# Kernel optimization log

Measured on AMD Instinct MI355X. Metric: run time of the kernel, lower is better.

Reference implementation:

```python
import jax, jax.numpy as jnp
import numpy as np

N_USERS = 100000
N_ITEMS = 40000
DIM = 64
NNZ_UI = 1500000
NNZ_II = 1000000
NNZ_UU = 1500000
UI_LAYERS = 3
ITEM_LAYERS = 2
USER_LAYERS = 2
EPS = 1e-12


def spmm(rows, cols, vals, x, n_rows):
    # sparse COO matrix (rows, cols, vals) @ dense x -> [n_rows, d]
    return jax.ops.segment_sum(vals[:, None] * x[cols], rows, num_segments=n_rows)


def l2_normalize(x):
    # matches F.normalize(x, p=2, dim=1) with eps clamp
    n = jnp.linalg.norm(x, axis=1, keepdims=True)
    return x / jnp.maximum(n, EPS)


def setup_inputs() -> dict:
    key = jax.random.key(0)
    ks = jax.random.split(key, 13)
    N = N_USERS + N_ITEMS
    return {
        "user_ui_emb": jax.random.normal(ks[0], (N_USERS, DIM), jnp.float32) * 0.1,
        "item_ui_emb": jax.random.normal(ks[1], (N_ITEMS, DIM), jnp.float32) * 0.1,
        "uu_emb": jax.random.normal(ks[2], (N_USERS, DIM), jnp.float32) * 0.1,
        "ii_emb": jax.random.normal(ks[3], (N_ITEMS, DIM), jnp.float32) * 0.1,
        "ui_vals": jax.random.uniform(ks[4], (NNZ_UI,), jnp.float32) / 12.0,
        "ii_vals": jax.random.uniform(ks[5], (NNZ_II,), jnp.float32) / 25.0,
        "uu_vals": jax.random.uniform(ks[6], (NNZ_UU,), jnp.float32) / 15.0,
        "ui_rows": jax.random.randint(ks[7], (NNZ_UI,), 0, N, jnp.int32),
        "ui_cols": jax.random.randint(ks[8], (NNZ_UI,), 0, N, jnp.int32),
        "ii_rows": jax.random.randint(ks[9], (NNZ_II,), 0, N_ITEMS, jnp.int32),
        "ii_cols": jax.random.randint(ks[10], (NNZ_II,), 0, N_ITEMS, jnp.int32),
        "uu_rows": jax.random.randint(ks[11], (NNZ_UU,), 0, N_USERS, jnp.int32),
        "uu_cols": jax.random.randint(ks[12], (NNZ_UU,), 0, N_USERS, jnp.int32),
    }


def reference(user_ui_emb, item_ui_emb, uu_emb, ii_emb,
              ui_vals, ii_vals, uu_vals,
              ui_rows, ui_cols, ii_rows, ii_cols, uu_rows, uu_cols):
    N = N_USERS + N_ITEMS
    # II propagation (item_loss_ratio != 0)
    ii = ii_emb
    for _ in range(ITEM_LAYERS):
        ii = spmm(ii_rows, ii_cols, ii_vals, ii, N_ITEMS)
    # UU propagation (user_loss_ratio != 0)
    uu = uu_emb
    for _ in range(USER_LAYERS):
        uu = spmm(uu_rows, uu_cols, uu_vals, uu, N_USERS)
    # LightGCN UI propagation
    ego = jnp.concatenate([user_ui_emb, item_ui_emb], axis=0)  # [N, d]
    acc = ego
    for _ in range(UI_LAYERS):
        ego = spmm(ui_rows, ui_cols, ui_vals, ego, N)
        acc = acc + ego
    all_emb = acc / (UI_LAYERS + 1)  # mean over stacked layers
    u_ui_emb = all_emb[:N_USERS]
    i_ui_emb = all_emb[N_USERS:]
    i_ui_emb = i_ui_emb + l2_normalize(ii)
    u_ui_emb = u_ui_emb + l2_normalize(uu)
    return (u_ui_emb, i_ui_emb, ii, uu)
```

## Files before the change

kernel.cpp:

```cpp
#include <hip/hip_runtime.h>

#define N_USERS_C 100000
#define N_ITEMS_C 40000
#define NTOT_C    140000
#define DIM_C     64
#define CDIV(a, b) (((a) + (b) - 1) / (b))

__device__ __forceinline__ unsigned short f2bf(float f) {
    unsigned u = __float_as_uint(f);
    unsigned r = (u + 0x7FFFu + ((u >> 16) & 1u)) >> 16;
    return (unsigned short)r;
}


template <int LOG_BR>
__global__ __launch_bounds__(256) void bucket_hist(
    const int* __restrict__ rows, int row_off, int* __restrict__ bkt_count,
    int nnz, int NB) {
    __shared__ int cnt[256];
    if (threadIdx.x < NB) cnt[threadIdx.x] = 0;
    __syncthreads();
    for (int e = blockIdx.x * 256 + threadIdx.x; e < nnz; e += gridDim.x * 256)
        atomicAdd(&cnt[(rows[e] + row_off) >> LOG_BR], 1);
    __syncthreads();
    if (threadIdx.x < NB) {
        int c = cnt[threadIdx.x];
        if (c) atomicAdd(&bkt_count[threadIdx.x], c);
    }
}

__global__ __launch_bounds__(256) void bucket_scan(
    const int* __restrict__ bkt_count, int* __restrict__ bkt_start,
    int* __restrict__ bkt_cursor, int NB, int nnz) {
    __shared__ int s[256];
    int v = (threadIdx.x < NB) ? bkt_count[threadIdx.x] : 0;
    s[threadIdx.x] = v;
    __syncthreads();
    #pragma unroll
    for (int off = 1; off < 256; off <<= 1) {
        int t = (threadIdx.x >= off) ? s[threadIdx.x - off] : 0;
        __syncthreads();
        s[threadIdx.x] += t;
        __syncthreads();
    }
    if (threadIdx.x < NB) {
        int ex = s[threadIdx.x] - v;
        bkt_start[threadIdx.x] = ex;
        bkt_cursor[threadIdx.x] = ex;
    }
    if (threadIdx.x == 0) bkt_start[NB] = nnz;
}

template <int LOG_BR>
__global__ __launch_bounds__(256) void partition_edges(
    const int* __restrict__ rows, const int* __restrict__ cols,
    const float* __restrict__ vals, int row_off, int col_off,
    int* __restrict__ bkt_cursor, int2* __restrict__ inter, int nnz) {
    __shared__ int cnt[256];
    __shared__ int base[256];
    const int tile = blockIdx.x * 4096;
    cnt[threadIdx.x] = 0;
    __syncthreads();
    int myrow[16];
    #pragma unroll
    for (int i = 0; i < 16; ++i) {
        int e = tile + i * 256 + threadIdx.x;
        int r = (e < nnz) ? (rows[e] + row_off) : -1;
        myrow[i] = r;
        if (r >= 0) atomicAdd(&cnt[r >> LOG_BR], 1);
    }
    __syncthreads();
    {
        int c = cnt[threadIdx.x];
        if (c) base[threadIdx.x] = atomicAdd(&bkt_cursor[threadIdx.x], c);
        cnt[threadIdx.x] = 0;
    }
    __syncthreads();
    #pragma unroll
    for (int i = 0; i < 16; ++i) {
        int r = myrow[i];
        if (r < 0) continue;
        int b = r >> LOG_BR;
        int rank = atomicAdd(&cnt[b], 1);
        int e = tile + i * 256 + threadIdx.x;
        int rl = r & ((1 << LOG_BR) - 1);
        inter[base[b] + rank] = make_int2((rl << 18) | (cols[e] + col_off),
                                          __float_as_int(vals[e]));
    }
}

template <int LOG_BR, int THREADS>
__global__ __launch_bounds__(THREADS) void bucket_to_csr(
    const int* __restrict__ bkt_start, const int2* __restrict__ inter,
    int2* __restrict__ spack, int* __restrict__ rowptr, int n_rows, int nnz) {
    const int BR = 1 << LOG_BR;
    const int C = BR / THREADS;
    __shared__ int hist[BR];
    __shared__ int bsum[THREADS];
    const int b = blockIdx.x;
    const int lo = bkt_start[b], hi = bkt_start[b + 1];
    #pragma unroll
    for (int j = 0; j < C; ++j) hist[threadIdx.x * C + j] = 0;
    __syncthreads();
    for (int i = lo + threadIdx.x; i < hi; i += THREADS)
        atomicAdd(&hist[inter[i].x >> 18], 1);
    __syncthreads();
    int loc[4];
    int sum = 0;
    #pragma unroll
    for (int j = 0; j < C; ++j) { loc[j] = sum; sum += hist[threadIdx.x * C + j]; }
    bsum[threadIdx.x] = sum;
    __syncthreads();
    #pragma unroll
    for (int off = 1; off < THREADS; off <<= 1) {
        int t = (threadIdx.x >= off) ? bsum[threadIdx.x - off] : 0;
        __syncthreads();
        bsum[threadIdx.x] += t;
        __syncthreads();
    }
    int texcl = bsum[threadIdx.x] - sum;
    __syncthreads();
    #pragma unroll
    for (int j = 0; j < C; ++j) {
        int r = threadIdx.x * C + j;
        int abs0 = lo + texcl + loc[j];
        int grow = (b << LOG_BR) + r;
        if (grow < n_rows) rowptr[grow] = abs0;
        hist[r] = abs0;
    }
    if (b == gridDim.x - 1 && threadIdx.x == 0) rowptr[n_rows] = nnz;
    __syncthreads();
    for (int i = lo + threadIdx.x; i < hi; i += THREADS) {
        int2 p = inter[i];
        int pos = atomicAdd(&hist[p.x >> 18], 1);
        spack[pos] = make_int2(p.x & 0x3FFFF, p.y);
    }
}

__global__ __launch_bounds__(256) void concat2_to_bf16(
    const float* __restrict__ A, const float* __restrict__ B, int n4A,
    int n4tot, unsigned short* __restrict__ dst) {
    int gid = blockIdx.x * blockDim.x + threadIdx.x;
    if (gid >= n4tot) return;
    float4 v = (gid < n4A) ? ((const float4*)A)[gid] : ((const float4*)B)[gid - n4A];
    ushort4 o;
    o.x = f2bf(v.x); o.y = f2bf(v.y); o.z = f2bf(v.z); o.w = f2bf(v.w);
    ((ushort4*)dst)[gid] = o;
}

template <int MODE>
__global__ __launch_bounds__(256, 6) void spmm_csr4(
    const int* __restrict__ rowptr, const int2* __restrict__ spack,
    const unsigned short* __restrict__ x, unsigned short* __restrict__ out_bf,
    float* __restrict__ out_f32, float* __restrict__ acc,
    const float* __restrict__ ego_u, const float* __restrict__ ego_i,
    int n_rows, int nnz) {
    const int wq   = (blockIdx.x * 256 + threadIdx.x) >> 6;
    const int lane = threadIdx.x & 63;
    const int l    = lane & 15;
    const int row  = wq * 4 + (lane >> 4);

    int j = rowptr[row];
    int e = rowptr[row + 1];
    int rem = e - j;
    int m1 = max(rem, __shfl_xor(rem, 16, 64));
    int mrem = max(m1, __shfl_xor(m1, 32, 64));

    const uint2* __restrict__ xq = (const uint2*)x;
    const int last = nnz - 1;

    float4 sa[4];
    #pragma unroll
    for (int u = 0; u < 4; ++u) sa[u] = make_float4(0.f, 0.f, 0.f, 0.f);

    if (mrem > 0) {
        int base = j;
        int2 pA[4], pB[4];
        #pragma unroll
        for (int u = 0; u < 4; ++u) pA[u] = spack[min(base + u, last)];
        #pragma unroll
        for (int u = 0; u < 4; ++u) pB[u] = spack[min(base + 4 + u, last)];
        uint2 gA[4], gB[4];
        #pragma unroll
        for (int u = 0; u < 4; ++u)
            gA[u] = xq[(u < rem) ? ((pA[u].x << 4) + l) : l];
        for (;;) {
            {
                int remN = rem - 4;
                #pragma unroll
                for (int u = 0; u < 4; ++u)
                    gB[u] = xq[(u < remN) ? ((pB[u].x << 4) + l) : l];
                float v[4];
                #pragma unroll
                for (int u = 0; u < 4; ++u)
                    v[u] = (u < rem) ? __int_as_float(pA[u].y) : 0.f;
                #pragma unroll
                for (int u = 0; u < 4; ++u)
                    pA[u] = spack[min(base + 8 + u, last)];
                #pragma unroll
                for (int u = 0; u < 4; ++u) {
                    sa[u].x += v[u] * __uint_as_float(gA[u].x << 16);
                    sa[u].y += v[u] * __uint_as_float(gA[u].x & 0xFFFF0000u);
                    sa[u].z += v[u] * __uint_as_float(gA[u].y << 16);
                    sa[u].w += v[u] * __uint_as_float(gA[u].y & 0xFFFF0000u);
                }
            }
            mrem -= 4;
            if (mrem <= 0) break;
            rem -= 4;
            base += 4;
            {
                int remN = rem - 4;
                #pragma unroll
                for (int u = 0; u < 4; ++u)
                    gA[u] = xq[(u < remN) ? ((pA[u].x << 4) + l) : l];
                float v[4];
                #pragma unroll
                for (int u = 0; u < 4; ++u)
                    v[u] = (u < rem) ? __int_as_float(pB[u].y) : 0.f;
                #pragma unroll
                for (int u = 0; u < 4; ++u)
                    pB[u] = spack[min(base + 8 + u, last)];
                #pragma unroll
                for (int u = 0; u < 4; ++u) {
                    sa[u].x += v[u] * __uint_as_float(gB[u].x << 16);
                    sa[u].y += v[u] * __uint_as_float(gB[u].x & 0xFFFF0000u);
                    sa[u].z += v[u] * __uint_as_float(gB[u].y << 16);
                    sa[u].w += v[u] * __uint_as_float(gB[u].y & 0xFFFF0000u);
                }
            }
            mrem -= 4;
            if (mrem <= 0) break;
            rem -= 4;
            base += 4;
        }
    }
    float4 s;
    s.x = (sa[0].x + sa[1].x) + (sa[2].x + sa[3].x);
    s.y = (sa[0].y + sa[1].y) + (sa[2].y + sa[3].y);
    s.z = (sa[0].z + sa[1].z) + (sa[2].z + sa[3].z);
    s.w = (sa[0].w + sa[1].w) + (sa[2].w + sa[3].w);

    const size_t idx4 = (size_t)row * 16 + l;
    if (MODE == 0 || MODE == 1 || MODE == 2) {
        ushort4 o;
        o.x = f2bf(s.x); o.y = f2bf(s.y); o.z = f2bf(s.z); o.w = f2bf(s.w);
        ((ushort4*)out_bf)[idx4] = o;
    }
    if (MODE == 1) {
        float4 e4 = (row < N_USERS_C)
            ? ((const float4*)ego_u)[idx4]
            : ((const float4*)ego_i)[(size_t)(row - N_USERS_C) * 16 + l];
        ((float4*)acc)[idx4] = make_float4(e4.x + s.x, e4.y + s.y,
                                           e4.z + s.z, e4.w + s.w);
    } else if (MODE == 2 || MODE == 3) {
        float4 a = ((const float4*)acc)[idx4];
        ((float4*)acc)[idx4] = make_float4(a.x + s.x, a.y + s.y,
                                           a.z + s.z, a.w + s.w);
    } else if (MODE == 4 || MODE == 5) {
        ((float4*)out_f32)[idx4] = s;
        float ss = s.x * s.x + s.y * s.y + s.z * s.z + s.w * s.w;
        #pragma unroll
        for (int off = 1; off < 16; off <<= 1) ss += __shfl_xor(ss, off, 64);
        float inv = 1.f / fmaxf(sqrtf(ss), 1e-12f);
        size_t aidx = idx4;
        if (MODE == 5) {
            int arow = (row < N_ITEMS_C) ? (N_USERS_C + row) : (row - N_ITEMS_C);
            aidx = (size_t)arow * 16 + l;
        }
        float4 a = ((const float4*)acc)[aidx];
        a.x = a.x * 0.25f + s.x * inv;
        a.y = a.y * 0.25f + s.y * inv;
        a.z = a.z * 0.25f + s.z * inv;
        a.w = a.w * 0.25f + s.w * inv;
        ((float4*)acc)[aidx] = a;
    }
}


template <int MODE>
static inline void run_spmm(const int* rowptr, const int2* spack,
                            const unsigned short* x, unsigned short* out_bf,
                            float* out_f32, float* acc, const float* ego_u,
                            const float* ego_i, int n_rows, int nnz, hipStream_t s) {
    spmm_csr4<MODE><<<n_rows / 16, 256, 0, s>>>(rowptr, spack, x, out_bf, out_f32,
                                                acc, ego_u, ego_i, n_rows, nnz);
}

extern "C" void kernel_launch(void* const* d_in, const int* in_sizes, int n_in,
                              void* d_out, int out_size, void* d_ws, size_t ws_size,
                              hipStream_t stream) {
    const float* user_ui = (const float*)d_in[0];
    const float* item_ui = (const float*)d_in[1];
    const float* uu_emb  = (const float*)d_in[2];
    const float* ii_emb  = (const float*)d_in[3];
    const float* ui_vals = (const float*)d_in[4];
    const float* ii_vals = (const float*)d_in[5];
    const float* uu_vals = (const float*)d_in[6];
    const int* ui_rows = (const int*)d_in[7];
    const int* ui_cols = (const int*)d_in[8];
    const int* ii_rows = (const int*)d_in[9];
    const int* ii_cols = (const int*)d_in[10];
    const int* uu_rows = (const int*)d_in[11];
    const int* uu_cols = (const int*)d_in[12];
    const int nnz_ui = in_sizes[4];
    const int nnz_ii = in_sizes[5];
    const int nnz_uu = in_sizes[6];
    const int nnz_cat = nnz_ii + nnz_uu;

    float* out    = (float*)d_out;
    float* acc    = out;
    float* acc_u  = acc;
    float* acc_i  = acc + (size_t)N_USERS_C * DIM_C;
    float* out_ii = out + (size_t)NTOT_C * DIM_C;
    float* out_uu = out_ii + (size_t)N_ITEMS_C * DIM_C;
    float* out_cat = out_ii;

    const size_t buf_bytes = (size_t)NTOT_C * DIM_C * sizeof(unsigned short);
    const size_t sp_ui  = (size_t)nnz_ui * sizeof(int2);
    const size_t sp_cat = (size_t)nnz_cat * sizeof(int2);
    const size_t meta_bytes = ((size_t)(NTOT_C + 1) + 1024) * sizeof(int);

    size_t slotA = sp_cat > sp_ui ? sp_cat : sp_ui;
    size_t slotB = slotA > buf_bytes ? slotA : buf_bytes;
    bool use_cat = ws_size >= slotA + slotB + buf_bytes + meta_bytes;
    if (!use_cat) {
        size_t mx = sp_ui;
        if ((size_t)nnz_ii * sizeof(int2) > mx) mx = (size_t)nnz_ii * sizeof(int2);
        if ((size_t)nnz_uu * sizeof(int2) > mx) mx = (size_t)nnz_uu * sizeof(int2);
        slotA = mx;
        slotB = buf_bytes;
    }

    char* p = (char*)d_ws;
    int2* spack = (int2*)p;                     p += slotA;
    int2* inter = (int2*)p;
    unsigned short* buf0 = (unsigned short*)p;  p += slotB;
    unsigned short* buf1 = (unsigned short*)p;  p += buf_bytes;
    int* rowptr     = (int*)p;
    int* bkt_count  = rowptr + (NTOT_C + 1);
    int* bkt_start  = bkt_count + 257;
    int* bkt_cursor = bkt_start + 258;

    const int n4tot = NTOT_C * DIM_C / 4;
    const int n4u   = N_USERS_C * DIM_C / 4;
    const int n4i   = N_ITEMS_C * DIM_C / 4;

    {
        const int NB = (NTOT_C + 1023) >> 10;
        hipMemsetAsync(bkt_count, 0, (size_t)NB * sizeof(int), stream);
        bucket_hist<10><<<512, 256, 0, stream>>>(ui_rows, 0, bkt_count, nnz_ui, NB);
        bucket_scan<<<1, 256, 0, stream>>>(bkt_count, bkt_start, bkt_cursor, NB, nnz_ui);
        partition_edges<10><<<(nnz_ui + 4095) / 4096, 256, 0, stream>>>(
            ui_rows, ui_cols, ui_vals, 0, 0, bkt_cursor, inter, nnz_ui);
        bucket_to_csr<10, 1024><<<NB, 1024, 0, stream>>>(bkt_start, inter, spack,
                                                         rowptr, NTOT_C, nnz_ui);
    }
    concat2_to_bf16<<<(n4tot + 255) / 256, 256, 0, stream>>>(user_ui, item_ui,
                                                             n4u, n4tot, buf1);
    run_spmm<1>(rowptr, spack, buf1, buf0, nullptr, acc, user_ui, item_ui,
                NTOT_C, nnz_ui, stream);
    run_spmm<2>(rowptr, spack, buf0, buf1, nullptr, acc, nullptr, nullptr,
                NTOT_C, nnz_ui, stream);
    run_spmm<3>(rowptr, spack, buf1, nullptr, nullptr, acc, nullptr, nullptr,
                NTOT_C, nnz_ui, stream);

    if (use_cat) {
        const int NB = (NTOT_C + 1023) >> 10;
        hipMemsetAsync(bkt_count, 0, (size_t)NB * sizeof(int), stream);
        bucket_hist<10><<<512, 256, 0, stream>>>(ii_rows, 0, bkt_count, nnz_ii, NB);
        bucket_hist<10><<<512, 256, 0, stream>>>(uu_rows, N_ITEMS_C, bkt_count,
                                                 nnz_uu, NB);
        bucket_scan<<<1, 256, 0, stream>>>(bkt_count, bkt_start, bkt_cursor, NB,
                                           nnz_cat);
        partition_edges<10><<<(nnz_ii + 4095) / 4096, 256, 0, stream>>>(
            ii_rows, ii_cols, ii_vals, 0, 0, bkt_cursor, inter, nnz_ii);
        partition_edges<10><<<(nnz_uu + 4095) / 4096, 256, 0, stream>>>(
            uu_rows, uu_cols, uu_vals, N_ITEMS_C, N_ITEMS_C, bkt_cursor, inter,
            nnz_uu);
        bucket_to_csr<10, 1024><<<NB, 1024, 0, stream>>>(bkt_start, inter, spack,
                                                         rowptr, NTOT_C, nnz_cat);
        concat2_to_bf16<<<(n4tot + 255) / 256, 256, 0, stream>>>(ii_emb, uu_emb,
                                                                 n4i, n4tot, buf1);
        run_spmm<0>(rowptr, spack, buf1, buf0, nullptr, nullptr, nullptr, nullptr,
                    NTOT_C, nnz_cat, stream);
        run_spmm<5>(rowptr, spack, buf0, nullptr, out_cat, acc, nullptr, nullptr,
                    NTOT_C, nnz_cat, stream);
    } else {
        {
            const int NB = (N_ITEMS_C + 255) >> 8;
            hipMemsetAsync(bkt_count, 0, (size_t)NB * sizeof(int), stream);
            bucket_hist<8><<<512, 256, 0, stream>>>(ii_rows, 0, bkt_count, nnz_ii, NB);
            bucket_scan<<<1, 256, 0, stream>>>(bkt_count, bkt_start, bkt_cursor,
                                               NB, nnz_ii);
            partition_edges<8><<<(nnz_ii + 4095) / 4096, 256, 0, stream>>>(
                ii_rows, ii_cols, ii_vals, 0, 0, bkt_cursor, inter, nnz_ii);
            bucket_to_csr<8, 256><<<NB, 256, 0, stream>>>(bkt_start, inter, spack,
                                                          rowptr, N_ITEMS_C, nnz_ii);
        }
        concat2_to_bf16<<<(n4i + 255) / 256, 256, 0, stream>>>(ii_emb, ii_emb,
                                                               n4i, n4i, buf0);
        run_spmm<0>(rowptr, spack, buf0, buf1, nullptr, nullptr, nullptr, nullptr,
                    N_ITEMS_C, nnz_ii, stream);
        run_spmm<4>(rowptr, spack, buf1, nullptr, out_ii, acc_i, nullptr, nullptr,
                    N_ITEMS_C, nnz_ii, stream);
        {
            const int NB = (N_USERS_C + 511) >> 9;
            hipMemsetAsync(bkt_count, 0, (size_t)NB * sizeof(int), stream);
            bucket_hist<9><<<512, 256, 0, stream>>>(uu_rows, 0, bkt_count, nnz_uu, NB);
            bucket_scan<<<1, 256, 0, stream>>>(bkt_count, bkt_start, bkt_cursor,
                                               NB, nnz_uu);
            partition_edges<9><<<(nnz_uu + 4095) / 4096, 256, 0, stream>>>(
                uu_rows, uu_cols, uu_vals, 0, 0, bkt_cursor, inter, nnz_uu);
            bucket_to_csr<9, 256><<<NB, 256, 0, stream>>>(bkt_start, inter, spack,
                                                          rowptr, N_USERS_C, nnz_uu);
        }
        concat2_to_bf16<<<(n4u + 255) / 256, 256, 0, stream>>>(uu_emb, uu_emb,
                                                               n4u, n4u, buf0);
        run_spmm<0>(rowptr, spack, buf0, buf1, nullptr, nullptr, nullptr, nullptr,
                    N_USERS_C, nnz_uu, stream);
        run_spmm<4>(rowptr, spack, buf1, nullptr, out_uu, acc_u, nullptr, nullptr,
                    N_USERS_C, nnz_uu, stream);
    }
}
```

Baseline: 613.7 us.

## Sort rows by degree for SpMM wave balance and pad edge array to drop clamps

Adds a degree histogram and scatter pass that builds a permutation ordering rows by descending degree (capped at 255). The SpMM kernel then maps each 16-lane group to a permuted row, so the four rows sharing a wavefront have similar lengths and less divergence from the max-remaining loop. It also zero-pads the packed edge array so the per-load min clamps and masked gather indices can be removed. The cost is extra small kernels per graph build, an indirect row lookup, and scattered output writes.

After: 1.458 ms. 2.38x slower.

```diff
diff --git a/kernel.cpp b/kernel.cpp
--- a/kernel.cpp
+++ b/kernel.cpp
@@ -4,6 +4,7 @@
 #define N_ITEMS_C 40000
 #define NTOT_C    140000
 #define DIM_C     64
+#define SPAD      256
 #define CDIV(a, b) (((a) + (b) - 1) / (b))
 
 __device__ __forceinline__ unsigned short f2bf(float f) {
@@ -137,6 +138,30 @@
     }
 }
 
+__global__ __launch_bounds__(256) void deg_hist(
+    const int* __restrict__ rowptr, int n, int* __restrict__ dhist) {
+    __shared__ int h[256];
+    h[threadIdx.x] = 0;
+    __syncthreads();
+    for (int i = blockIdx.x * 256 + threadIdx.x; i < n; i += gridDim.x * 256) {
+        int d = rowptr[i + 1] - rowptr[i];
+        atomicAdd(&h[255 - min(d, 255)], 1);
+    }
+    __syncthreads();
+    int c = h[threadIdx.x];
+    if (c) atomicAdd(&dhist[threadIdx.x], c);
+}
+
+__global__ __launch_bounds__(256) void deg_scatter(
+    const int* __restrict__ rowptr, int n, int* __restrict__ dcur,
+    int* __restrict__ perm) {
+    int i = blockIdx.x * 256 + threadIdx.x;
+    if (i >= n) return;
+    int d = rowptr[i + 1] - rowptr[i];
+    int pos = atomicAdd(&dcur[255 - min(d, 255)], 1);
+    perm[pos] = i;
+}
+
 __global__ __launch_bounds__(256) void concat2_to_bf16(
     const float* __restrict__ A, const float* __restrict__ B, int n4A,
     int n4tot, unsigned short* __restrict__ dst) {
@@ -150,15 +175,15 @@
 
 template <int MODE>
 __global__ __launch_bounds__(256, 6) void spmm_csr4(
-    const int* __restrict__ rowptr, const int2* __restrict__ spack,
-    const unsigned short* __restrict__ x, unsigned short* __restrict__ out_bf,
-    float* __restrict__ out_f32, float* __restrict__ acc,
-    const float* __restrict__ ego_u, const float* __restrict__ ego_i,
-    int n_rows, int nnz) {
+    const int* __restrict__ rowptr, const int* __restrict__ perm,
+    const int2* __restrict__ spack, const unsigned short* __restrict__ x,
+    unsigned short* __restrict__ out_bf, float* __restrict__ out_f32,
+    float* __restrict__ acc, const float* __restrict__ ego_u,
+    const float* __restrict__ ego_i) {
     const int wq   = (blockIdx.x * 256 + threadIdx.x) >> 6;
     const int lane = threadIdx.x & 63;
     const int l    = lane & 15;
-    const int row  = wq * 4 + (lane >> 4);
+    const int row  = perm[wq * 4 + (lane >> 4)];
 
     int j = rowptr[row];
     int e = rowptr[row + 1];
@@ -167,7 +192,6 @@
     int mrem = max(m1, __shfl_xor(m1, 32, 64));
 
     const uint2* __restrict__ xq = (const uint2*)x;
-    const int last = nnz - 1;
 
     float4 sa[4];
     #pragma unroll
@@ -177,26 +201,22 @@
         int base = j;
         int2 pA[4], pB[4];
         #pragma unroll
-        for (int u = 0; u < 4; ++u) pA[u] = spack[min(base + u, last)];
+        for (int u = 0; u < 4; ++u) pA[u] = spack[base + u];
         #pragma unroll
-        for (int u = 0; u < 4; ++u) pB[u] = spack[min(base + 4 + u, last)];
+        for (int u = 0; u < 4; ++u) pB[u] = spack[base + 4 + u];
         uint2 gA[4], gB[4];
         #pragma unroll
-        for (int u = 0; u < 4; ++u)
-            gA[u] = xq[(u < rem) ? ((pA[u].x << 4) + l) : l];
+        for (int u = 0; u < 4; ++u) gA[u] = xq[(pA[u].x << 4) + l];
         for (;;) {
             {
-                int remN = rem - 4;
-                #pragma unroll
-                for (int u = 0; u < 4; ++u)
-                    gB[u] = xq[(u < remN) ? ((pB[u].x << 4) + l) : l];
+                #pragma unroll
+                for (int u = 0; u < 4; ++u) gB[u] = xq[(pB[u].x << 4) + l];
                 float v[4];
                 #pragma unroll
                 for (int u = 0; u < 4; ++u)
                     v[u] = (u < rem) ? __int_as_float(pA[u].y) : 0.f;
                 #pragma unroll
-                for (int u = 0; u < 4; ++u)
-                    pA[u] = spack[min(base + 8 + u, last)];
+                for (int u = 0; u < 4; ++u) pA[u] = spack[base + 8 + u];
                 #pragma unroll
                 for (int u = 0; u < 4; ++u) {
                     sa[u].x += v[u] * __uint_as_float(gA[u].x << 16);
@@ -210,17 +230,14 @@
             rem -= 4;
             base += 4;
             {
-                int remN = rem - 4;
-                #pragma unroll
-                for (int u = 0; u < 4; ++u)
-                    gA[u] = xq[(u < remN) ? ((pA[u].x << 4) + l) : l];
+                #pragma unroll
+                for (int u = 0; u < 4; ++u) gA[u] = xq[(pA[u].x << 4) + l];
                 float v[4];
                 #pragma unroll
                 for (int u = 0; u < 4; ++u)
                     v[u] = (u < rem) ? __int_as_float(pB[u].y) : 0.f;
                 #pragma unroll
-                for (int u = 0; u < 4; ++u)
-                    pB[u] = spack[min(base + 8 + u, last)];
+                for (int u = 0; u < 4; ++u) pB[u] = spack[base + 8 + u];
                 #pragma unroll
                 for (int u = 0; u < 4; ++u) {
                     sa[u].x += v[u] * __uint_as_float(gB[u].x << 16);
@@ -279,12 +296,21 @@
 
 
 template <int MODE>
-static inline void run_spmm(const int* rowptr, const int2* spack,
-                            const unsigned short* x, unsigned short* out_bf,
-                            float* out_f32, float* acc, const float* ego_u,
-                            const float* ego_i, int n_rows, int nnz, hipStream_t s) {
-    spmm_csr4<MODE><<<n_rows / 16, 256, 0, s>>>(rowptr, spack, x, out_bf, out_f32,
-                                                acc, ego_u, ego_i, n_rows, nnz);
+static inline void run_spmm(const int* rowptr, const int* perm,
+                            const int2* spack, const unsigned short* x,
+                            unsigned short* out_bf, float* out_f32, float* acc,
+                            const float* ego_u, const float* ego_i, int n_rows,
+                            hipStream_t s) {
+    spmm_csr4<MODE><<<n_rows / 16, 256, 0, s>>>(rowptr, perm, spack, x, out_bf,
+                                                out_f32, acc, ego_u, ego_i);
+}
+
+static inline void build_perm(const int* rowptr, int n, int* dhist, int* dstart,
+                              int* dcur, int* perm, hipStream_t s) {
+    hipMemsetAsync(dhist, 0, 256 * sizeof(int), s);
+    deg_hist<<<256, 256, 0, s>>>(rowptr, n, dhist);
+    bucket_scan<<<1, 256, 0, s>>>(dhist, dstart, dcur, 256, n);
+    deg_scatter<<<CDIV(n, 256), 256, 0, s>>>(rowptr, n, dcur, perm);
 }
 
 extern "C" void kernel_launch(void* const* d_in, const int* in_sizes, int n_in,
@@ -319,16 +345,17 @@
     const size_t buf_bytes = (size_t)NTOT_C * DIM_C * sizeof(unsigned short);
     const size_t sp_ui  = (size_t)nnz_ui * sizeof(int2);
     const size_t sp_cat = (size_t)nnz_cat * sizeof(int2);
-    const size_t meta_bytes = ((size_t)(NTOT_C + 1) + 1024) * sizeof(int);
-
-    size_t slotA = sp_cat > sp_ui ? sp_cat : sp_ui;
+    const size_t pad_bytes = (size_t)SPAD * sizeof(int2);
+    const size_t meta_bytes = ((size_t)(NTOT_C + 1) + NTOT_C + 4096) * sizeof(int);
+
+    size_t slotA = (sp_cat > sp_ui ? sp_cat : sp_ui) + pad_bytes;
     size_t slotB = slotA > buf_bytes ? slotA : buf_bytes;
     bool use_cat = ws_size >= slotA + slotB + buf_bytes + meta_bytes;
     if (!use_cat) {
         size_t mx = sp_ui;
         if ((size_t)nnz_ii * sizeof(int2) > mx) mx = (size_t)nnz_ii * sizeof(int2);
         if ((size_t)nnz_uu * sizeof(int2) > mx) mx = (size_t)nnz_uu * sizeof(int2);
-        slotA = mx;
+        slotA = mx + pad_bytes;
         slotB = buf_bytes;
     }
 
@@ -341,6 +368,10 @@
     int* bkt_count  = rowptr + (NTOT_C + 1);
     int* bkt_start  = bkt_count + 257;
     int* bkt_cursor = bkt_start + 258;
+    int* perm       = bkt_cursor + 257;
+    int* dhist      = perm + NTOT_C;
+    int* dstart     = dhist + 256;
+    int* dcur       = dstart + 257;
 
     const int n4tot = NTOT_C * DIM_C / 4;
     const int n4u   = N_USERS_C * DIM_C / 4;
@@ -355,15 +386,17 @@
             ui_rows, ui_cols, ui_vals, 0, 0, bkt_cursor, inter, nnz_ui);
         bucket_to_csr<10, 1024><<<NB, 1024, 0, stream>>>(bkt_start, inter, spack,
                                                          rowptr, NTOT_C, nnz_ui);
+        hipMemsetAsync(spack + nnz_ui, 0, pad_bytes, stream);
+        build_perm(rowptr, NTOT_C, dhist, dstart, dcur, perm, stream);
     }
     concat2_to_bf16<<<(n4tot + 255) / 256, 256, 0, stream>>>(user_ui, item_ui,
                                                              n4u, n4tot, buf1);
-    run_spmm<1>(rowptr, spack, buf1, buf0, nullptr, acc, user_ui, item_ui,
-                NTOT_C, nnz_ui, stream);
-    run_spmm<2>(rowptr, spack, buf0, buf1, nullptr, acc, nullptr, nullptr,
-                NTOT_C, nnz_ui, stream);
-    run_spmm<3>(rowptr, spack, buf1, nullptr, nullptr, acc, nullptr, nullptr,
-                NTOT_C, nnz_ui, stream);
+    run_spmm<1>(rowptr, perm, spack, buf1, buf0, nullptr, acc, user_ui, item_ui,
+                NTOT_C, stream);
+    run_spmm<2>(rowptr, perm, spack, buf0, buf1, nullptr, acc, nullptr, nullptr,
+                NTOT_C, stream);
+    run_spmm<3>(rowptr, perm, spack, buf1, nullptr, nullptr, acc, nullptr, nullptr,
+                NTOT_C, stream);
 
     if (use_cat) {
         const int NB = (NTOT_C + 1023) >> 10;
@@ -380,12 +413,14 @@
             nnz_uu);
         bucket_to_csr<10, 1024><<<NB, 1024, 0, stream>>>(bkt_start, inter, spack,
                                                          rowptr, NTOT_C, nnz_cat);
+        hipMemsetAsync(spack + nnz_cat, 0, pad_bytes, stream);
+        build_perm(rowptr, NTOT_C, dhist, dstart, dcur, perm, stream);
         concat2_to_bf16<<<(n4tot + 255) / 256, 256, 0, stream>>>(ii_emb, uu_emb,
                                                                  n4i, n4tot, buf1);
-        run_spmm<0>(rowptr, spack, buf1, buf0, nullptr, nullptr, nullptr, nullptr,
-                    NTOT_C, nnz_cat, stream);
-        run_spmm<5>(rowptr, spack, buf0, nullptr, out_cat, acc, nullptr, nullptr,
-                    NTOT_C, nnz_cat, stream);
+        run_spmm<0>(rowptr, perm, spack, buf1, buf0, nullptr, nullptr, nullptr,
+                    nullptr, NTOT_C, stream);
+        run_spmm<5>(rowptr, perm, spack, buf0, nullptr, out_cat, acc, nullptr,
+                    nullptr, NTOT_C, stream);
     } else {
         {
             const int NB = (N_ITEMS_C + 255) >> 8;
@@ -397,13 +432,15 @@
                 ii_rows, ii_cols, ii_vals, 0, 0, bkt_cursor, inter, nnz_ii);
             bucket_to_csr<8, 256><<<NB, 256, 0, stream>>>(bkt_start, inter, spack,
                                                           rowptr, N_ITEMS_C, nnz_ii);
+            hipMemsetAsync(spack + nnz_ii, 0, pad_bytes, stream);
+            build_perm(rowptr, N_ITEMS_C, dhist, dstart, dcur, perm, stream);
         }
         concat2_to_bf16<<<(n4i + 255) / 256, 256, 0, stream>>>(ii_emb, ii_emb,
                                                                n4i, n4i, buf0);
-        run_spmm<0>(rowptr, spack, buf0, buf1, nullptr, nullptr, nullptr, nullptr,
-                    N_ITEMS_C, nnz_ii, stream);
-        run_spmm<4>(rowptr, spack, buf1, nullptr, out_ii, acc_i, nullptr, nullptr,
-                    N_ITEMS_C, nnz_ii, stream);
+        run_spmm<0>(rowptr, perm, spack, buf0, buf1, nullptr, nullptr, nullptr,
+                    nullptr, N_ITEMS_C, stream);
+        run_spmm<4>(rowptr, perm, spack, buf1, nullptr, out_ii, acc_i, nullptr,
+                    nullptr, N_ITEMS_C, stream);
         {
             const int NB = (N_USERS_C + 511) >> 9;
             hipMemsetAsync(bkt_count, 0, (size_t)NB * sizeof(int), stream);
@@ -414,12 +451,14 @@
                 uu_rows, uu_cols, uu_vals, 0, 0, bkt_cursor, inter, nnz_uu);
             bucket_to_csr<9, 256><<<NB, 256, 0, stream>>>(bkt_start, inter, spack,
                                                           rowptr, N_USERS_C, nnz_uu);
+            hipMemsetAsync(spack + nnz_uu, 0, pad_bytes, stream);
+            build_perm(rowptr, N_USERS_C, dhist, dstart, dcur, perm, stream);
         }
         concat2_to_bf16<<<(n4u + 255) / 256, 256, 0, stream>>>(uu_emb, uu_emb,
                                                                n4u, n4u, buf0);
-        run_spmm<0>(rowptr, spack, buf0, buf1, nullptr, nullptr, nullptr, nullptr,
-                    N_USERS_C, nnz_uu, stream);
-        run_spmm<4>(rowptr, spack, buf1, nullptr, out_uu, acc_u, nullptr, nullptr,
-                    N_USERS_C, nnz_uu, stream);
-    }
-}
+        run_spmm<0>(rowptr, perm, spack, buf0, buf1, nullptr, nullptr, nullptr,
+                    nullptr, N_USERS_C, stream);
+        run_spmm<4>(rowptr, perm, spack, buf1, nullptr, out_uu, acc_u, nullptr,
+                    nullptr, N_USERS_C, stream);
+    }
+}
```
